# Optimization experiments

Measured on AMD Instinct MI355X. Metric: run time of the kernel, lower is better.

## Reference

```python
import jax, jax.numpy as jnp
import numpy as np
from jax import lax

INPUT = 78   # 26 * 3
HID = 4
L, B = 2048, 512


def _lstm_layer(x, W_ih, W_hh, b_ih, b_hh):
    """Single unidirectional LSTM layer, PyTorch gate order (i, f, g, o).
    x: [L, B, D] -> [L, B, H]"""
    H = W_hh.shape[1]
    Bsz = x.shape[1]
    # Precompute input contribution for all timesteps: [L, B, 4H]
    xg = jnp.einsum('lbd,gd->lbg', x, W_ih) + b_ih + b_hh

    def step(carry, xg_t):
        h, c = carry
        gates = xg_t + h @ W_hh.T  # [B, 4H]
        i, f, g, o = jnp.split(gates, 4, axis=-1)
        i = jax.nn.sigmoid(i)
        f = jax.nn.sigmoid(f)
        g = jnp.tanh(g)
        o = jax.nn.sigmoid(o)
        c = f * c + i * g
        h = o * jnp.tanh(c)
        return (h, c), h

    h0 = jnp.zeros((Bsz, H), x.dtype)
    c0 = jnp.zeros((Bsz, H), x.dtype)
    _, ys = lax.scan(step, (h0, c0), xg)
    return ys  # [L, B, H]


def setup_inputs() -> dict:
    key = jax.random.key(0)
    ks = jax.random.split(key, 10)
    x = jax.random.normal(ks[0], (L, B, INPUT), dtype=jnp.float32)
    lens = jax.random.randint(ks[1], (B,), 1, L + 1)  # in [1, L]
    s = 1.0 / np.sqrt(HID)
    def u(k, shape):
        return jax.random.uniform(k, shape, jnp.float32, -s, s)
    return {
        'x': x,
        'lens': lens,
        'W_ih0': u(ks[2], (4 * HID, INPUT)),
        'W_hh0': u(ks[3], (4 * HID, HID)),
        'b_ih0': u(ks[4], (4 * HID,)),
        'b_hh0': u(ks[5], (4 * HID,)),
        'W_ih1': u(ks[6], (4 * HID, HID)),
        'W_hh1': u(ks[7], (4 * HID, HID)),
        'b_ih1': u(ks[8], (4 * HID,)),
        'b_hh1': u(ks[9], (4 * HID,)),
    }


def reference(x, lens, W_ih0, W_hh0, b_ih0, b_hh0, W_ih1, W_hh1, b_ih1, b_hh1):
    # 2-layer unidirectional LSTM over padded input. Because the LSTM is causal,
    # outputs at valid positions (t < len) equal those of the packed computation;
    # we zero out positions t >= len to match packed semantics (pad_packed form).
    y0 = _lstm_layer(x, W_ih0, W_hh0, b_ih0, b_hh0)
    y1 = _lstm_layer(y0, W_ih1, W_hh1, b_ih1, b_hh1)
    mask = (jnp.arange(x.shape[0])[:, None] < lens[None, :])[:, :, None]
    return jnp.where(mask, y1, 0.0)  # [L, B, HID]
```

## Files before the change

kernel.cpp:

```cpp
#include <hip/hip_runtime.h>


#define LSEQ  2048
#define BATCH 512
#define NIN   78
#define LOG2E 1.4426950408889634f

#define WS_BIAS_F  0
#define WS_XG_F    5120
#define XG_BYTES   ((unsigned)LSEQ * BATCH * 16u * 4u)

#define RPB  128
#define TPB1 128

__device__ __forceinline__ float rcp_(float x) { return __builtin_amdgcn_rcpf(x); }
__device__ __forceinline__ float ex2_(float x) { return __builtin_amdgcn_exp2f(x); }

template<int CTRL>
__device__ __forceinline__ float dppf(float x) {
  int r = __builtin_amdgcn_update_dpp(0, __builtin_bit_cast(int, x), CTRL, 0xf, 0xf, false);
  return __builtin_bit_cast(float, r);
}
template<int PAT>
__device__ __forceinline__ float swzf(float x) {
  int r = __builtin_amdgcn_ds_swizzle(__builtin_bit_cast(int, x), PAT);
  return __builtin_bit_cast(float, r);
}

__global__ __launch_bounds__(TPB1) void xg_kernel(
    const float* __restrict__ x, const float* __restrict__ Wih0,
    const float* __restrict__ bih0, const float* __restrict__ bhh0,
    const float* __restrict__ bih1, const float* __restrict__ bhh1,
    float* __restrict__ ws)
{
  __shared__ float xs[RPB * NIN];
  const int tid = threadIdx.x;
  const int r0  = blockIdx.x * RPB;

  if (blockIdx.x == 0 && tid < 16) {
    const int j = tid >> 2, g = tid & 3, row = j + 4 * g;
    const float s = (g == 2) ? 2.f * LOG2E : -LOG2E;
    ws[WS_BIAS_F + tid] = s * (bih1[row] + bhh1[row]);
  }

  const float4* gx = (const float4*)(x + (size_t)r0 * NIN);
  float4* ls = (float4*)xs;
  for (int i = tid; i < RPB * NIN / 4; i += TPB1) ls[i] = gx[i];
  __syncthreads();

  const float* xr = xs + tid * NIN;
  float acc[16];
#pragma unroll
  for (int row = 0; row < 16; ++row) acc[row] = bih0[row] + bhh0[row];
  for (int k = 0; k < NIN; ++k) {
    const float xk = xr[k];
#pragma unroll
    for (int row = 0; row < 16; ++row) acc[row] += xk * Wih0[row * NIN + k];
  }
#pragma unroll
  for (int row = 0; row < 16; ++row) {
    const float s = ((row >> 2) == 2) ? 2.f * LOG2E : -LOG2E;
    acc[row] *= s;
  }
  float* o = ws + WS_XG_F + (size_t)(r0 + tid) * 16;
#pragma unroll
  for (int j = 0; j < 4; ++j) {
    float4 v = make_float4(acc[j], acc[j + 4], acc[j + 8], acc[j + 12]);
    *(float4*)(o + j * 4) = v;
  }
}

__global__ __launch_bounds__(64) void lstm_rec(
    const float* __restrict__ wsr,
    const int* __restrict__ lens,
    const float* __restrict__ Whh0, const float* __restrict__ Whh1,
    const float* __restrict__ Wih1,
    float* __restrict__ out)
{
  const int lane  = threadIdx.x;
  const int g     = lane & 3;
  const int j     = (lane >> 2) & 3;
  const int layer = (lane >> 4) & 1;
  const int b     = blockIdx.x * 2 + (lane >> 5);

  const float sg = (g == 2) ? 2.f * LOG2E : -LOG2E;
  const float ka = (g == 2) ? -4.f * LOG2E : 1.f;
  const float kb = (g == 2) ?  2.f * LOG2E : 0.f;

  const int row4 = (g * 4 + j) * 4;
  const float* whh = layer ? Whh1 : Whh0;
  float wA[4], wB[4];
#pragma unroll
  for (int m = 0; m < 4; ++m) {
    wA[m] = sg * whh[row4 + (j ^ m)];
    wB[m] = layer ? sg * Wih1[row4 + (j ^ m)] : 0.f;
  }
  const int len = lens[b];

  unsigned ofs = layer ? (unsigned)((j * 4 + g) * 4)
                       : (unsigned)(WS_XG_F * 4 + (b * 16 + j * 4 + g) * 4);
  const unsigned stride = layer ? 0u : (unsigned)(BATCH * 16 * 4);
  const unsigned maxofs = (unsigned)(WS_XG_F * 4) + XG_BYTES - 4u;

  float* sp = out + b * 4 + j;

  float A0 = 0.f, A1 = 0.f, A2 = 0.f, A3 = 0.f;
  float B0 = 0.f, B1 = 0.f, B2 = 0.f, B3 = 0.f;
  float cs = 0.f;

  auto ld1 = [&](unsigned o) -> float {
    o = (o > maxofs) ? maxofs : o;
    return *(const float*)((const char*)wsr + o);
  };

  float buf[8];
#pragma unroll
  for (int p = 0; p < 8; ++p) { buf[p] = ld1(ofs); ofs += stride; }

  auto step = [&](const float base, int t, bool do_store) {
    float p0 = fmaf(A0, wA[0], base);
    p0 = fmaf(A1, wA[1], p0);
    float p1 = A2 * wA[2];
    p1 = fmaf(A3, wA[3], p1);
    float p2 = fmaf(B0, wB[0], B1 * wB[1]);
    float p3 = fmaf(B2, wB[2], B3 * wB[3]);
    const float P = (p0 + p1) + (p2 + p3);

    const float r   = rcp_(1.f + ex2_(P));
    const float act = fmaf(ka, r, kb);

    const float vi = dppf<0x00>(act), vf = dppf<0x55>(act),
                vg = dppf<0xAA>(act), vo = dppf<0xFF>(act);

    cs = fmaf(vf, cs, vi * vg);
    const float tc = fmaf(-2.f, rcp_(1.f + ex2_(cs)), 1.f);
    const float hq = vo * tc;

    A0 = hq;
    A1 = swzf<0x101F>(hq);
    A2 = swzf<0x201F>(hq);
    A3 = swzf<0x301F>(hq);
    B0 = swzf<0x401F>(hq);
    B1 = swzf<0x501F>(hq);
    B2 = swzf<0x601F>(hq);
    B3 = swzf<0x701F>(hq);

    if (do_store) {
      if (layer && g == 0) *sp = (t < len) ? hq : 0.f;
      sp += BATCH * 4;
    }
  };

  step(buf[0], -1, false);
  if (layer) { cs = 0.f; A0 = 0.f; A1 = 0.f; A2 = 0.f; A3 = 0.f; }
  buf[0] = ld1(ofs); ofs += stride;

#pragma unroll 8
  for (int k = 1; k <= LSEQ; ++k) {
    step(buf[k & 7], k - 1, true);
    buf[k & 7] = ld1(ofs); ofs += stride;
  }
}

extern "C" void kernel_launch(void* const* d_in, const int* in_sizes, int n_in,
                              void* d_out, int out_size, void* d_ws, size_t ws_size,
                              hipStream_t stream) {
  const float* x    = (const float*)d_in[0];
  const int*   lens = (const int*)d_in[1];
  const float* Wih0 = (const float*)d_in[2];
  const float* Whh0 = (const float*)d_in[3];
  const float* bih0 = (const float*)d_in[4];
  const float* bhh0 = (const float*)d_in[5];
  const float* Wih1 = (const float*)d_in[6];
  const float* Whh1 = (const float*)d_in[7];
  const float* bih1 = (const float*)d_in[8];
  const float* bhh1 = (const float*)d_in[9];
  float* ws  = (float*)d_ws;
  float* out = (float*)d_out;

  xg_kernel<<<(LSEQ * BATCH) / RPB, TPB1, 0, stream>>>(
      x, Wih0, bih0, bhh0, bih1, bhh1, ws);
  lstm_rec<<<BATCH / 2, 64, 0, stream>>>(
      ws, lens, Whh0, Whh1, Wih1, out);
}
```

Measured before the change: 772.4 us.

## Skew layer-1 two steps behind layer-0 and use DPP for intra-quad broadcast

Layer 0 now runs two timesteps ahead of layer 1, with double-buffered cross-layer inputs (Bb0/Bb1). Each layer-0 output is therefore consumed two steps later, so the cross-layer ds_swizzle latency is off the per-step dependency chain. The three intra-row swizzles that broadcast h across the j lanes are replaced by DPP row_half_mirror, row_mirror and quad-permute ops, which are expected to have lower latency than LDS-based swizzles. This adds a second warm-up step and a more complex loop, and it relies on the clamped reads past the end of xg.

```diff
diff --git a/kernel.cpp b/kernel.cpp
--- a/kernel.cpp
+++ b/kernel.cpp
@@ -26,6 +26,10 @@
   int r = __builtin_amdgcn_ds_swizzle(__builtin_bit_cast(int, x), PAT);
   return __builtin_bit_cast(float, r);
 }
+
+#define QP_REV  0x1B
+#define ROW_HM  0x141
+#define ROW_MIR 0x140
 
 __global__ __launch_bounds__(TPB1) void xg_kernel(
     const float* __restrict__ x, const float* __restrict__ Wih0,
@@ -105,7 +109,8 @@
   float* sp = out + b * 4 + j;
 
   float A0 = 0.f, A1 = 0.f, A2 = 0.f, A3 = 0.f;
-  float B0 = 0.f, B1 = 0.f, B2 = 0.f, B3 = 0.f;
+  float Bb0[4] = {0.f, 0.f, 0.f, 0.f};
+  float Bb1[4] = {0.f, 0.f, 0.f, 0.f};
   float cs = 0.f;
 
   auto ld1 = [&](unsigned o) -> float {
@@ -117,14 +122,15 @@
 #pragma unroll
   for (int p = 0; p < 8; ++p) { buf[p] = ld1(ofs); ofs += stride; }
 
-  auto step = [&](const float base, int t, bool do_store) {
-    float p0 = fmaf(A0, wA[0], base);
-    p0 = fmaf(A1, wA[1], p0);
-    float p1 = A2 * wA[2];
-    p1 = fmaf(A3, wA[3], p1);
-    float p2 = fmaf(B0, wB[0], B1 * wB[1]);
-    float p3 = fmaf(B2, wB[2], B3 * wB[3]);
-    const float P = (p0 + p1) + (p2 + p3);
+  auto step = [&](const float base, float (&B)[4], int t, bool do_store) {
+    float pre = fmaf(B[0], wB[0], base);
+    pre = fmaf(B[1], wB[1], pre);
+    float pre2 = fmaf(B[3], wB[3], B[2] * wB[2]);
+    pre += pre2;
+
+    float m01 = fmaf(A1, wA[1], A0 * wA[0]);
+    float m23 = fmaf(A3, wA[3], A2 * wA[2]);
+    const float P = (m01 + m23) + pre;
 
     const float r   = rcp_(1.f + ex2_(P));
     const float act = fmaf(ka, r, kb);
@@ -136,14 +142,17 @@
     const float tc = fmaf(-2.f, rcp_(1.f + ex2_(cs)), 1.f);
     const float hq = vo * tc;
 
+    const float hm_ = dppf<ROW_HM>(hq);
+    const float rm_ = dppf<ROW_MIR>(hq);
     A0 = hq;
-    A1 = swzf<0x101F>(hq);
-    A2 = swzf<0x201F>(hq);
-    A3 = swzf<0x301F>(hq);
-    B0 = swzf<0x401F>(hq);
-    B1 = swzf<0x501F>(hq);
-    B2 = swzf<0x601F>(hq);
-    B3 = swzf<0x701F>(hq);
+    A1 = dppf<QP_REV>(hm_);
+    A2 = dppf<ROW_HM>(rm_);
+    A3 = dppf<QP_REV>(rm_);
+
+    B[0] = swzf<0x401F>(A0);
+    B[1] = swzf<0x401F>(A1);
+    B[2] = swzf<0x401F>(A2);
+    B[3] = swzf<0x401F>(A3);
 
     if (do_store) {
       if (layer && g == 0) *sp = (t < len) ? hq : 0.f;
@@ -151,14 +160,18 @@
     }
   };
 
-  step(buf[0], -1, false);
+  step(buf[0], Bb0, -2, false); buf[0] = ld1(ofs); ofs += stride;
+  step(buf[1], Bb1, -1, false); buf[1] = ld1(ofs); ofs += stride;
   if (layer) { cs = 0.f; A0 = 0.f; A1 = 0.f; A2 = 0.f; A3 = 0.f; }
-  buf[0] = ld1(ofs); ofs += stride;
 
-#pragma unroll 8
-  for (int k = 1; k <= LSEQ; ++k) {
-    step(buf[k & 7], k - 1, true);
-    buf[k & 7] = ld1(ofs); ofs += stride;
+  int t = 0;
+#pragma unroll 4
+  for (int i = 2; i < LSEQ + 2; i += 2) {
+    step(buf[i & 7], Bb0, t, true);
+    buf[i & 7] = ld1(ofs); ofs += stride;
+    step(buf[(i + 1) & 7], Bb1, t + 1, true);
+    buf[(i + 1) & 7] = ld1(ofs); ofs += stride;
+    t += 2;
   }
 }
 
```

After: 797.0 us. +3.2%, slower.

## Restructure input-projection kernel with LDS-staged weights, packed FMA, two rows per thread

Applied to the files above, without the earlier changes.

The input-projection kernel now uses 64 threads per block, each computing two rows. The pre-scaled, transposed Wih0 is staged in shared memory instead of being read from global memory per element. The inner product uses packed two-wide FMAs (v_pk_fma_f32), and the gate scaling is folded into the weights and bias. The aim is to cut per-element global weight loads and halve FMA instruction count in the xg phase. In exchange there are fewer threads per block and higher register pressure. The recurrent kernel, which probably dominates the runtime, is unchanged.

```diff
diff --git a/kernel.cpp b/kernel.cpp
--- a/kernel.cpp
+++ b/kernel.cpp
@@ -11,10 +11,14 @@
 #define XG_BYTES   ((unsigned)LSEQ * BATCH * 16u * 4u)
 
 #define RPB  128
-#define TPB1 128
+
+typedef __attribute__((ext_vector_type(2))) float vf2;
 
 __device__ __forceinline__ float rcp_(float x) { return __builtin_amdgcn_rcpf(x); }
 __device__ __forceinline__ float ex2_(float x) { return __builtin_amdgcn_exp2f(x); }
+__device__ __forceinline__ vf2 pkfma(vf2 a, vf2 b, vf2 c) {
+  return __builtin_elementwise_fma(a, b, c);
+}
 
 template<int CTRL>
 __device__ __forceinline__ float dppf(float x) {
@@ -27,13 +31,14 @@
   return __builtin_bit_cast(float, r);
 }
 
-__global__ __launch_bounds__(TPB1) void xg_kernel(
+__global__ __launch_bounds__(64) void xg_kernel(
     const float* __restrict__ x, const float* __restrict__ Wih0,
     const float* __restrict__ bih0, const float* __restrict__ bhh0,
     const float* __restrict__ bih1, const float* __restrict__ bhh1,
     float* __restrict__ ws)
 {
   __shared__ float xs[RPB * NIN];
+  __shared__ float wT[NIN][16];
   const int tid = threadIdx.x;
   const int r0  = blockIdx.x * RPB;
 
@@ -43,30 +48,69 @@
     ws[WS_BIAS_F + tid] = s * (bih1[row] + bhh1[row]);
   }
 
+  for (int i = tid; i < NIN * 16; i += 64) {
+    const int k = i >> 4, a = i & 15;
+    const int j = a >> 2, g = a & 3;
+    const float s = (g == 2) ? 2.f * LOG2E : -LOG2E;
+    wT[k][a] = s * Wih0[(g * 4 + j) * NIN + k];
+  }
+
   const float4* gx = (const float4*)(x + (size_t)r0 * NIN);
   float4* ls = (float4*)xs;
-  for (int i = tid; i < RPB * NIN / 4; i += TPB1) ls[i] = gx[i];
+#pragma unroll
+  for (int i = 0; i < (RPB * NIN / 4) / 64; ++i)
+    ls[tid + i * 64] = gx[tid + i * 64];
   __syncthreads();
 
-  const float* xr = xs + tid * NIN;
-  float acc[16];
-#pragma unroll
-  for (int row = 0; row < 16; ++row) acc[row] = bih0[row] + bhh0[row];
-  for (int k = 0; k < NIN; ++k) {
-    const float xk = xr[k];
-#pragma unroll
-    for (int row = 0; row < 16; ++row) acc[row] += xk * Wih0[row * NIN + k];
-  }
-#pragma unroll
-  for (int row = 0; row < 16; ++row) {
-    const float s = ((row >> 2) == 2) ? 2.f * LOG2E : -LOG2E;
-    acc[row] *= s;
-  }
-  float* o = ws + WS_XG_F + (size_t)(r0 + tid) * 16;
-#pragma unroll
-  for (int j = 0; j < 4; ++j) {
-    float4 v = make_float4(acc[j], acc[j + 4], acc[j + 8], acc[j + 12]);
-    *(float4*)(o + j * 4) = v;
+  vf2 accA[8], accB[8];
+#pragma unroll
+  for (int p = 0; p < 8; ++p) {
+    float bv[2];
+#pragma unroll
+    for (int u = 0; u < 2; ++u) {
+      const int a = 2 * p + u, j = a >> 2, g = a & 3;
+      const float s = (g == 2) ? 2.f * LOG2E : -LOG2E;
+      bv[u] = s * (bih0[g * 4 + j] + bhh0[g * 4 + j]);
+    }
+    accA[p] = vf2{ bv[0], bv[1] };
+    accB[p] = vf2{ bv[0], bv[1] };
+  }
+
+  const float* xrA = xs + tid * NIN;
+  const float* xrB = xs + (tid + 64) * NIN;
+
+#pragma unroll 3
+  for (int k2 = 0; k2 < NIN / 2; ++k2) {
+    const vf2 xA2 = *(const vf2*)(xrA + 2 * k2);
+    const vf2 xB2 = *(const vf2*)(xrB + 2 * k2);
+    const float4* wk0 = (const float4*)&wT[2 * k2][0];
+    const float4* wk1 = (const float4*)&wT[2 * k2 + 1][0];
+    const vf2 xa0 = vf2{ xA2.x, xA2.x }, xa1 = vf2{ xA2.y, xA2.y };
+    const vf2 xb0 = vf2{ xB2.x, xB2.x }, xb1 = vf2{ xB2.y, xB2.y };
+#pragma unroll
+    for (int q = 0; q < 4; ++q) {
+      const float4 w0 = wk0[q], w1 = wk1[q];
+      const vf2 w0a = vf2{ w0.x, w0.y }, w0b = vf2{ w0.z, w0.w };
+      const vf2 w1a = vf2{ w1.x, w1.y }, w1b = vf2{ w1.z, w1.w };
+      accA[2 * q]     = pkfma(xa0, w0a, accA[2 * q]);
+      accA[2 * q + 1] = pkfma(xa0, w0b, accA[2 * q + 1]);
+      accA[2 * q]     = pkfma(xa1, w1a, accA[2 * q]);
+      accA[2 * q + 1] = pkfma(xa1, w1b, accA[2 * q + 1]);
+      accB[2 * q]     = pkfma(xb0, w0a, accB[2 * q]);
+      accB[2 * q + 1] = pkfma(xb0, w0b, accB[2 * q + 1]);
+      accB[2 * q]     = pkfma(xb1, w1a, accB[2 * q]);
+      accB[2 * q + 1] = pkfma(xb1, w1b, accB[2 * q + 1]);
+    }
+  }
+
+  float* oA = ws + WS_XG_F + (size_t)(r0 + tid) * 16;
+  float* oB = ws + WS_XG_F + (size_t)(r0 + 64 + tid) * 16;
+#pragma unroll
+  for (int q = 0; q < 4; ++q) {
+    *(float4*)(oA + q * 4) = make_float4(accA[2 * q].x, accA[2 * q].y,
+                                         accA[2 * q + 1].x, accA[2 * q + 1].y);
+    *(float4*)(oB + q * 4) = make_float4(accB[2 * q].x, accB[2 * q].y,
+                                         accB[2 * q + 1].x, accB[2 * q + 1].y);
   }
 }
 
@@ -178,7 +222,7 @@
   float* ws  = (float*)d_ws;
   float* out = (float*)d_out;
 
-  xg_kernel<<<(LSEQ * BATCH) / RPB, TPB1, 0, stream>>>(
+  xg_kernel<<<(LSEQ * BATCH) / RPB, 64, 0, stream>>>(
       x, Wih0, bih0, bhh0, bih1, bhh1, ws);
   lstm_rec<<<BATCH / 2, 64, 0, stream>>>(
       ws, lens, Whh0, Whh1, Wih1, out);
```

Result: faster. 716.0 us (-7.3%).

## Fuse input projection into recurrent kernel with producer waves and LDS progress flags

Applied to the files above, without the earlier changes.

The separate input-projection kernel and recurrent kernel are merged into one 320-thread block per batch pair. Four producer waves compute the layer-0 input gates for that block's two sequences in chunks of 8 timesteps, write them to the workspace, and publish progress counters in shared memory. The recurrent wave polls those counters before consuming each chunk, so the projection overlaps the serial recurrence instead of running as a separate kernel first. Layer-1 bias is now folded in directly rather than read from the workspace. The risks are polling overhead and latency on the critical path. The producers also read x with scalar global loads and hold 78 weights in registers, which may add register pressure.

```diff
diff --git a/kernel.cpp b/kernel.cpp
--- a/kernel.cpp
+++ b/kernel.cpp
@@ -6,12 +6,8 @@
 #define NIN   78
 #define LOG2E 1.4426950408889634f
 
-#define WS_BIAS_F  0
 #define WS_XG_F    5120
 #define XG_BYTES   ((unsigned)LSEQ * BATCH * 16u * 4u)
-
-#define RPB  128
-#define TPB1 128
 
 __device__ __forceinline__ float rcp_(float x) { return __builtin_amdgcn_rcpf(x); }
 __device__ __forceinline__ float ex2_(float x) { return __builtin_amdgcn_exp2f(x); }
@@ -27,61 +23,65 @@
   return __builtin_bit_cast(float, r);
 }
 
-__global__ __launch_bounds__(TPB1) void xg_kernel(
-    const float* __restrict__ x, const float* __restrict__ Wih0,
+__global__ __launch_bounds__(320) void lstm_fused(
+    const float* __restrict__ x,
+    const int* __restrict__ lens,
+    const float* __restrict__ Wih0, const float* __restrict__ Whh0,
     const float* __restrict__ bih0, const float* __restrict__ bhh0,
+    const float* __restrict__ Wih1, const float* __restrict__ Whh1,
     const float* __restrict__ bih1, const float* __restrict__ bhh1,
-    float* __restrict__ ws)
+    float* __restrict__ ws, float* __restrict__ out)
 {
-  __shared__ float xs[RPB * NIN];
-  const int tid = threadIdx.x;
-  const int r0  = blockIdx.x * RPB;
-
-  if (blockIdx.x == 0 && tid < 16) {
-    const int j = tid >> 2, g = tid & 3, row = j + 4 * g;
+  __shared__ unsigned long long progq;
+  const int tid  = threadIdx.x;
+  const int wave = tid >> 6;
+  const int lane = tid & 63;
+  if (tid == 0) progq = 0ull;
+  __syncthreads();
+  const int b0 = blockIdx.x * 2;
+
+  if (wave != 0) {
+    const int w   = wave;
+    const int a   = lane & 15;
+    const int grp = lane >> 4;
+    const int dt  = grp >> 1, db = grp & 1;
+    const int j   = a >> 2, g = a & 3;
     const float s = (g == 2) ? 2.f * LOG2E : -LOG2E;
-    ws[WS_BIAS_F + tid] = s * (bih1[row] + bhh1[row]);
+    const int row = g * 4 + j;
+
+    float wr[NIN];
+#pragma unroll
+    for (int k = 0; k < NIN; ++k) wr[k] = s * Wih0[row * NIN + k];
+    const float bias0 = s * (bih0[row] + bhh0[row]);
+
+    const int b = b0 + db;
+    float* __restrict__ xg = ws + WS_XG_F;
+    volatile unsigned short* pr = (volatile unsigned short*)&progq;
+
+    for (int p = 0; p < LSEQ / 8; ++p) {
+      const int t = 8 * p + 2 * (w - 1) + dt;
+      const float* __restrict__ xr = x + ((size_t)t * BATCH + b) * NIN;
+      float a0 = bias0, a1 = 0.f, a2 = 0.f, a3 = 0.f;
+#pragma unroll
+      for (int k = 0; k < 76; k += 4) {
+        a0 = fmaf(xr[k],     wr[k],     a0);
+        a1 = fmaf(xr[k + 1], wr[k + 1], a1);
+        a2 = fmaf(xr[k + 2], wr[k + 2], a2);
+        a3 = fmaf(xr[k + 3], wr[k + 3], a3);
+      }
+      a0 = fmaf(xr[76], wr[76], a0);
+      a1 = fmaf(xr[77], wr[77], a1);
+      xg[((size_t)t * BATCH + b) * 16 + a] = (a0 + a1) + (a2 + a3);
+      __threadfence_block();
+      if (lane == 0) pr[w - 1] = (unsigned short)(p + 1);
+    }
+    return;
   }
 
-  const float4* gx = (const float4*)(x + (size_t)r0 * NIN);
-  float4* ls = (float4*)xs;
-  for (int i = tid; i < RPB * NIN / 4; i += TPB1) ls[i] = gx[i];
-  __syncthreads();
-
-  const float* xr = xs + tid * NIN;
-  float acc[16];
-#pragma unroll
-  for (int row = 0; row < 16; ++row) acc[row] = bih0[row] + bhh0[row];
-  for (int k = 0; k < NIN; ++k) {
-    const float xk = xr[k];
-#pragma unroll
-    for (int row = 0; row < 16; ++row) acc[row] += xk * Wih0[row * NIN + k];
-  }
-#pragma unroll
-  for (int row = 0; row < 16; ++row) {
-    const float s = ((row >> 2) == 2) ? 2.f * LOG2E : -LOG2E;
-    acc[row] *= s;
-  }
-  float* o = ws + WS_XG_F + (size_t)(r0 + tid) * 16;
-#pragma unroll
-  for (int j = 0; j < 4; ++j) {
-    float4 v = make_float4(acc[j], acc[j + 4], acc[j + 8], acc[j + 12]);
-    *(float4*)(o + j * 4) = v;
-  }
-}
-
-__global__ __launch_bounds__(64) void lstm_rec(
-    const float* __restrict__ wsr,
-    const int* __restrict__ lens,
-    const float* __restrict__ Whh0, const float* __restrict__ Whh1,
-    const float* __restrict__ Wih1,
-    float* __restrict__ out)
-{
-  const int lane  = threadIdx.x;
   const int g     = lane & 3;
   const int j     = (lane >> 2) & 3;
   const int layer = (lane >> 4) & 1;
-  const int b     = blockIdx.x * 2 + (lane >> 5);
+  const int b     = b0 + (lane >> 5);
 
   const float sg = (g == 2) ? 2.f * LOG2E : -LOG2E;
   const float ka = (g == 2) ? -4.f * LOG2E : 1.f;
@@ -97,7 +97,10 @@
   }
   const int len = lens[b];
 
-  unsigned ofs = layer ? (unsigned)((j * 4 + g) * 4)
+  const float keep = layer ? 0.f : 1.f;
+  const float badd = layer ? sg * (bih1[g * 4 + j] + bhh1[g * 4 + j]) : 0.f;
+
+  unsigned ofs = layer ? (unsigned)(WS_XG_F * 4)
                        : (unsigned)(WS_XG_F * 4 + (b * 16 + j * 4 + g) * 4);
   const unsigned stride = layer ? 0u : (unsigned)(BATCH * 16 * 4);
   const unsigned maxofs = (unsigned)(WS_XG_F * 4) + XG_BYTES - 4u;
@@ -108,16 +111,34 @@
   float B0 = 0.f, B1 = 0.f, B2 = 0.f, B3 = 0.f;
   float cs = 0.f;
 
+  const char* wsr = (const char*)ws;
   auto ld1 = [&](unsigned o) -> float {
     o = (o > maxofs) ? maxofs : o;
-    return *(const float*)((const char*)wsr + o);
+    return *(const float*)(wsr + o);
   };
 
-  float buf[8];
-#pragma unroll
-  for (int p = 0; p < 8; ++p) { buf[p] = ld1(ofs); ofs += stride; }
-
-  auto step = [&](const float base, int t, bool do_store) {
+  volatile unsigned long long* pq = &progq;
+  int avail = 0;
+  auto wait_t = [&](int need) {
+    if (avail >= need) return;
+    for (;;) {
+      const unsigned long long v = *pq;
+      unsigned v0 = (unsigned)(v & 0xffff);
+      unsigned v1 = (unsigned)((v >> 16) & 0xffff);
+      unsigned v2 = (unsigned)((v >> 32) & 0xffff);
+      unsigned v3 = (unsigned)((v >> 48) & 0xffff);
+      unsigned m01 = v0 < v1 ? v0 : v1;
+      unsigned m23 = v2 < v3 ? v2 : v3;
+      unsigned mn  = m01 < m23 ? m01 : m23;
+      avail = (int)(8u * mn);
+      if (avail >= need) break;
+      __builtin_amdgcn_s_sleep(8);
+    }
+    asm volatile("" ::: "memory");
+  };
+
+  auto step = [&](const float bufv, int t, bool do_store) {
+    const float base = fmaf(keep, bufv, badd);
     float p0 = fmaf(A0, wA[0], base);
     p0 = fmaf(A1, wA[1], p0);
     float p1 = A2 * wA[2];
@@ -151,14 +172,24 @@
     }
   };
 
+  wait_t(16);
+  float buf[8];
+#pragma unroll
+  for (int p = 0; p < 8; ++p) { buf[p] = ld1(ofs); ofs += stride; }
   step(buf[0], -1, false);
   if (layer) { cs = 0.f; A0 = 0.f; A1 = 0.f; A2 = 0.f; A3 = 0.f; }
   buf[0] = ld1(ofs); ofs += stride;
 
-#pragma unroll 8
-  for (int k = 1; k <= LSEQ; ++k) {
-    step(buf[k & 7], k - 1, true);
-    buf[k & 7] = ld1(ofs); ofs += stride;
+  for (int wi = 0; wi < LSEQ / 8; ++wi) {
+    int need = 8 * wi + 24;
+    if (need > LSEQ) need = LSEQ;
+    wait_t(need);
+#pragma unroll
+    for (int kk = 0; kk < 8; ++kk) {
+      const int k = 8 * wi + 1 + kk;
+      step(buf[(1 + kk) & 7], k - 1, true);
+      buf[(1 + kk) & 7] = ld1(ofs); ofs += stride;
+    }
   }
 }
 
@@ -178,8 +209,6 @@
   float* ws  = (float*)d_ws;
   float* out = (float*)d_out;
 
-  xg_kernel<<<(LSEQ * BATCH) / RPB, TPB1, 0, stream>>>(
-      x, Wih0, bih0, bhh0, bih1, bhh1, ws);
-  lstm_rec<<<BATCH / 2, 64, 0, stream>>>(
-      ws, lens, Whh0, Whh1, Wih1, out);
-}
+  lstm_fused<<<BATCH / 2, 320, 0, stream>>>(
+      x, lens, Wih0, Whh0, bih0, bhh0, Wih1, Whh1, bih1, bhh1, ws, out);
+}
```

New measurement: 1.020 ms. 32.0% more time.
